# Performance work log

Measured on AMD Instinct MI355X. Metric: run time of the kernel, lower is better.

Reference implementation:

```python
import jax, jax.numpy as jnp
import numpy as np

IN_FEATURES = 4096
OUT_FEATURES = 11008
GROUP_SIZE = 128
N_HIGH = 1024   # int(0.25*4096)//8*8
N_LOW = 3072    # (4096-1024)//8*8
M_TOKENS = 64


def unpack_6bit(packed, original_k):
    # packed: [K*3//4, N] uint8 values stored as int32
    _, N = packed.shape
    p = packed.reshape(original_k // 4, 3, N)
    b0, b1, b2 = p[:, 0], p[:, 1], p[:, 2]
    v0 = b0 & 63
    v1 = ((b0 >> 6) & 3) | ((b1 & 15) << 2)
    v2 = ((b1 >> 4) & 15) | ((b2 & 3) << 4)
    v3 = (b2 >> 2) & 63
    return jnp.stack([v0, v1, v2, v3], axis=1).reshape(original_k, N)


def unpack_5bit(packed, original_k):
    # packed: [K*5//8, N]
    _, N = packed.shape
    p = packed.reshape(original_k // 8, 5, N)
    b = [p[:, i] for i in range(5)]
    v0 = b[0] & 31
    v1 = ((b[0] >> 5) & 7) | ((b[1] & 3) << 3)
    v2 = (b[1] >> 2) & 31
    v3 = ((b[1] >> 7) & 1) | ((b[2] & 15) << 1)
    v4 = ((b[2] >> 4) & 15) | ((b[3] & 1) << 4)
    v5 = (b[3] >> 1) & 31
    v6 = ((b[3] >> 6) & 3) | ((b[4] & 7) << 2)
    v7 = (b[4] >> 3) & 31
    return jnp.stack([v0, v1, v2, v3, v4, v5, v6, v7], axis=1).reshape(original_k, N)


def dequant_region(W_q, scales, half_range):
    # W_q: [K, N] ints in [0, 2*half_range]; scales: [num_groups, N]
    K, N = W_q.shape
    G = scales.shape[0]
    Wg = (W_q.astype(jnp.float32) - float(half_range)).reshape(G, GROUP_SIZE, N)
    return (Wg * scales[:, None, :]).reshape(K, N)


def setup_inputs() -> dict:
    key = jax.random.key(0)
    ks = jax.random.split(key, 7)
    x = jax.random.normal(ks[0], (M_TOKENS, IN_FEATURES), dtype=jnp.float32)
    W_high_packed = jax.random.randint(ks[1], (N_HIGH * 3 // 4, OUT_FEATURES), 0, 256, dtype=jnp.int32)
    W_low_packed = jax.random.randint(ks[2], (N_LOW * 5 // 8, OUT_FEATURES), 0, 256, dtype=jnp.int32)
    scales_high = jax.random.uniform(ks[3], (N_HIGH // GROUP_SIZE, OUT_FEATURES), dtype=jnp.float32) * 0.02 + 1e-4
    scales_low = jax.random.uniform(ks[4], (N_LOW // GROUP_SIZE, OUT_FEATURES), dtype=jnp.float32) * 0.02 + 1e-4
    col_indices = jax.random.permutation(ks[5], IN_FEATURES).astype(jnp.int32)
    bias = jax.random.normal(ks[6], (OUT_FEATURES,), dtype=jnp.float32) * 0.02
    return {"x": x, "W_high_packed": W_high_packed, "W_low_packed": W_low_packed,
            "scales_high": scales_high, "scales_low": scales_low,
            "col_indices": col_indices, "bias": bias}


def reference(x, W_high_packed, W_low_packed, scales_high, scales_low, col_indices, bias):
    # Unpack mixed 6-bit / 5-bit weights and group-dequantize.
    Wq_high = unpack_6bit(W_high_packed, N_HIGH)          # [1024, N], 0..63
    Wq_low = unpack_5bit(W_low_packed, N_LOW)             # [3072, N], 0..31
    W_high = dequant_region(Wq_high, scales_high, 31)     # 6-bit half_range = 31
    W_low = dequant_region(Wq_low, scales_low, 15)        # 5-bit half_range = 15
    # Column-sensitivity reorder of activations, then split high/low regions.
    x_perm = x[:, col_indices]                            # [M, K]
    x_high = x_perm[:, :N_HIGH]
    x_low = x_perm[:, N_HIGH:N_HIGH + N_LOW]
    out = x_high @ W_high + x_low @ W_low + bias          # [M, N]
    return out
```

## Files before the change

kernel.cpp:

```cpp
#include <hip/hip_runtime.h>


#define NFEAT 11008
#define KTOT  4096

typedef _Float16 half8 __attribute__((ext_vector_type(8)));
typedef float    f32x4 __attribute__((ext_vector_type(4)));

#define GLOAD4(g, l)  __builtin_amdgcn_global_load_lds(                         \
    (const __attribute__((address_space(1))) unsigned int*)(g),                 \
    (__attribute__((address_space(3))) unsigned int*)(l), 4, 0, 0)
#define GLOAD16(g, l) __builtin_amdgcn_global_load_lds(                         \
    (const __attribute__((address_space(1))) unsigned int*)(g),                 \
    (__attribute__((address_space(3))) unsigned int*)(l), 16, 0, 0)
#define WAITV(N) asm volatile("s_waitcnt vmcnt(" #N ")" ::: "memory")

__global__ __launch_bounds__(256) void prep_xfrag(const float* __restrict__ x,
                                                  const int* __restrict__ col,
                                                  _Float16* __restrict__ xfrag) {
    int idx = blockIdx.x * 256 + threadIdx.x;
    int j  = idx & 7;
    int l  = (idx >> 3) & 63;
    int mt = (idx >> 9) & 3;
    int s  = idx >> 11;
    int k  = s * 32 + ((l >> 4) << 3) + j;
    int m  = mt * 16 + (l & 15);
    xfrag[idx] = (_Float16)x[m * KTOT + col[k]];
}

__global__ __launch_bounds__(256, 3) void gemm_kernel(const int* __restrict__ Wh,
                                                      const int* __restrict__ Wl,
                                                      const float* __restrict__ sh,
                                                      const float* __restrict__ sl,
                                                      const _Float16* __restrict__ xfrag,
                                                      float* __restrict__ dst,
                                                      int atomic_mode) {
    const int n0   = blockIdx.x * 64;
    const int kc   = blockIdx.y;
    const int lane = threadIdx.x & 63;
    const int wave = threadIdx.x >> 6;
    const int cb   = wave * 16 + (lane & 15);
    const int n    = n0 + cb;
    const int o    = lane >> 4;

    __shared__ int Wb[4][1632];
    __shared__ __align__(16) _Float16 Ab[4][4][512];

    f32x4 acc[4];
#pragma unroll
    for (int i = 0; i < 4; ++i) acc[i] = (f32x4){0.f, 0.f, 0.f, 0.f};

    if (kc == 0) {
        float sc[8];
#pragma unroll
        for (int g = 0; g < 8; ++g) sc[g] = sh[g * NFEAT + n];

#define STAGE6(T) do {                                                         \
        const int _t = (T); const int _b = _t & 3;                             \
        const int* _gs = Wh + (_t * 24 + wave * 6) * NFEAT + n0 + lane;        \
        GLOAD4(_gs,             &Wb[_b][(wave * 6 + 0) * 68]);                 \
        GLOAD4(_gs + 1 * NFEAT, &Wb[_b][(wave * 6 + 1) * 68]);                 \
        GLOAD4(_gs + 2 * NFEAT, &Wb[_b][(wave * 6 + 2) * 68]);                 \
        GLOAD4(_gs + 3 * NFEAT, &Wb[_b][(wave * 6 + 3) * 68]);                 \
        GLOAD4(_gs + 4 * NFEAT, &Wb[_b][(wave * 6 + 4) * 68]);                 \
        GLOAD4(_gs + 5 * NFEAT, &Wb[_b][(wave * 6 + 5) * 68]);                 \
        GLOAD16(xfrag + ((size_t)(_t * 4 + wave) * 64 + lane) * 8,             \
                &Ab[_b][wave][0]);                                             \
    } while (0)

        STAGE6(0);
        STAGE6(1);
#pragma unroll
        for (int g = 0; g < 8; ++g) {
            for (int st = 0; st < 4; ++st) {
                const int t = g * 4 + st;
                if (t + 2 < 32) { STAGE6(t + 2); WAITV(14); }
                else if (t + 1 < 32) { WAITV(7); }
                else { WAITV(0); }
                __builtin_amdgcn_s_barrier();
                asm volatile("" ::: "memory");

                const int  bi = t & 3;
                const int* wr = &Wb[bi][(o * 6) * 68 + cb];
                const int b0 = wr[0];      const int b1 = wr[68];
                const int b2 = wr[2 * 68]; const int b3 = wr[3 * 68];
                const int b4 = wr[4 * 68]; const int b5 = wr[5 * 68];
                int v0 = b0 & 63;
                int v1 = ((b0 >> 6) & 3) | ((b1 & 15) << 2);
                int v2 = ((b1 >> 4) & 15) | ((b2 & 3) << 4);
                int v3 = (b2 >> 2) & 63;
                int v4 = b3 & 63;
                int v5 = ((b3 >> 6) & 3) | ((b4 & 15) << 2);
                int v6 = ((b4 >> 4) & 15) | ((b5 & 3) << 4);
                int v7 = (b5 >> 2) & 63;
                const float s = sc[g], moff = -31.0f * sc[g];
                half8 bf;
                bf[0] = (_Float16)fmaf((float)v0, s, moff);
                bf[1] = (_Float16)fmaf((float)v1, s, moff);
                bf[2] = (_Float16)fmaf((float)v2, s, moff);
                bf[3] = (_Float16)fmaf((float)v3, s, moff);
                bf[4] = (_Float16)fmaf((float)v4, s, moff);
                bf[5] = (_Float16)fmaf((float)v5, s, moff);
                bf[6] = (_Float16)fmaf((float)v6, s, moff);
                bf[7] = (_Float16)fmaf((float)v7, s, moff);
#pragma unroll
                for (int mt = 0; mt < 4; ++mt) {
                    half8 a = *(const half8*)&Ab[bi][mt][lane * 8];
                    acc[mt] = __builtin_amdgcn_mfma_f32_16x16x32_f16(a, bf, acc[mt], 0, 0, 0);
                }
            }
        }
#undef STAGE6
    } else {
        const int klc   = kc - 1;
        const int rbase = klc * 640;
        float sc[8];
#pragma unroll
        for (int g = 0; g < 8; ++g) sc[g] = sl[(klc * 8 + g) * NFEAT + n];

#define STAGE5(T) do {                                                         \
        const int _t = (T); const int _b = _t & 3;                             \
        const int* _gs = Wl + (rbase + _t * 20 + wave * 5) * NFEAT + n0 + lane;\
        GLOAD4(_gs,             &Wb[_b][(wave * 5 + 0) * 72]);                 \
        GLOAD4(_gs + 1 * NFEAT, &Wb[_b][(wave * 5 + 1) * 72]);                 \
        GLOAD4(_gs + 2 * NFEAT, &Wb[_b][(wave * 5 + 2) * 72]);                 \
        GLOAD4(_gs + 3 * NFEAT, &Wb[_b][(wave * 5 + 3) * 72]);                 \
        GLOAD4(_gs + 4 * NFEAT, &Wb[_b][(wave * 5 + 4) * 72]);                 \
        GLOAD16(xfrag + ((size_t)((kc * 32 + _t) * 4 + wave) * 64 + lane) * 8, \
                &Ab[_b][wave][0]);                                             \
    } while (0)

        STAGE5(0);
        STAGE5(1);
#pragma unroll
        for (int g = 0; g < 8; ++g) {
            for (int st = 0; st < 4; ++st) {
                const int t = g * 4 + st;
                if (t + 2 < 32) { STAGE5(t + 2); WAITV(12); }
                else if (t + 1 < 32) { WAITV(6); }
                else { WAITV(0); }
                __builtin_amdgcn_s_barrier();
                asm volatile("" ::: "memory");

                const int  bi = t & 3;
                const int* wr = &Wb[bi][(o * 5) * 72 + cb];
                const int b0 = wr[0];      const int b1 = wr[72];
                const int b2 = wr[2 * 72]; const int b3 = wr[3 * 72];
                const int b4 = wr[4 * 72];
                int v0 = b0 & 31;
                int v1 = ((b0 >> 5) & 7) | ((b1 & 3) << 3);
                int v2 = (b1 >> 2) & 31;
                int v3 = ((b1 >> 7) & 1) | ((b2 & 15) << 1);
                int v4 = ((b2 >> 4) & 15) | ((b3 & 1) << 4);
                int v5 = (b3 >> 1) & 31;
                int v6 = ((b3 >> 6) & 3) | ((b4 & 7) << 2);
                int v7 = (b4 >> 3) & 31;
                const float s = sc[g], moff = -15.0f * sc[g];
                half8 bf;
                bf[0] = (_Float16)fmaf((float)v0, s, moff);
                bf[1] = (_Float16)fmaf((float)v1, s, moff);
                bf[2] = (_Float16)fmaf((float)v2, s, moff);
                bf[3] = (_Float16)fmaf((float)v3, s, moff);
                bf[4] = (_Float16)fmaf((float)v4, s, moff);
                bf[5] = (_Float16)fmaf((float)v5, s, moff);
                bf[6] = (_Float16)fmaf((float)v6, s, moff);
                bf[7] = (_Float16)fmaf((float)v7, s, moff);
#pragma unroll
                for (int mt = 0; mt < 4; ++mt) {
                    half8 a = *(const half8*)&Ab[bi][mt][lane * 8];
                    acc[mt] = __builtin_amdgcn_mfma_f32_16x16x32_f16(a, bf, acc[mt], 0, 0, 0);
                }
            }
        }
#undef STAGE5
    }

    const int r0 = (lane >> 4) << 2;
    if (atomic_mode) {
#pragma unroll
        for (int mt = 0; mt < 4; ++mt)
#pragma unroll
            for (int r = 0; r < 4; ++r)
                atomicAdd(&dst[(mt * 16 + r0 + r) * NFEAT + n], acc[mt][r]);
    } else {
        float* base = dst + (size_t)kc * 64 * NFEAT;
#pragma unroll
        for (int mt = 0; mt < 4; ++mt)
#pragma unroll
            for (int r = 0; r < 4; ++r)
                base[(mt * 16 + r0 + r) * NFEAT + n] = acc[mt][r];
    }
}

__global__ __launch_bounds__(256) void reduce_out(const float* __restrict__ part,
                                                  const float* __restrict__ bias,
                                                  float* __restrict__ out, int nc) {
    const int idx = blockIdx.x * 256 + threadIdx.x;
    const int f   = idx * 4;
    const int n   = f % NFEAT;
    f32x4 sum = *(const f32x4*)(bias + n);
    for (int c = 0; c < nc; ++c)
        sum += *(const f32x4*)(part + (size_t)c * 704512 + f);
    *(f32x4*)(out + f) = sum;
}

__global__ __launch_bounds__(256) void init_bias(const float* __restrict__ bias,
                                                 float* __restrict__ out) {
    const int idx = blockIdx.x * 256 + threadIdx.x;
    out[idx] = bias[idx % NFEAT];
}

extern "C" void kernel_launch(void* const* d_in, const int* in_sizes, int n_in,
                              void* d_out, int out_size, void* d_ws, size_t ws_size,
                              hipStream_t stream) {
    const float* x    = (const float*)d_in[0];
    const int*   Wh   = (const int*)d_in[1];
    const int*   Wl   = (const int*)d_in[2];
    const float* sh   = (const float*)d_in[3];
    const float* sl   = (const float*)d_in[4];
    const int*   col  = (const int*)d_in[5];
    const float* bias = (const float*)d_in[6];
    float* out = (float*)d_out;

    _Float16* xfrag = (_Float16*)d_ws;
    const size_t xfrag_bytes = 64 * KTOT * sizeof(_Float16);
    const size_t part1 = 64ull * NFEAT * sizeof(float);

    prep_xfrag<<<1024, 256, 0, stream>>>(x, col, xfrag);

    dim3 grid(172, 4);
    if (ws_size >= xfrag_bytes + 4 * part1) {
        float* part = (float*)((char*)d_ws + xfrag_bytes);
        gemm_kernel<<<grid, 256, 0, stream>>>(Wh, Wl, sh, sl, xfrag, part, 0);
        reduce_out<<<688, 256, 0, stream>>>(part, bias, out, 4);
    } else {
        init_bias<<<2752, 256, 0, stream>>>(bias, out);
        gemm_kernel<<<grid, 256, 0, stream>>>(Wh, Wl, sh, sl, xfrag, out, 1);
    }
}
```

Measured before the change: 173.0 us.

## Widen N tile to 128, use 16-byte LDS loads, split K into eight chunks

Each block now covers 128 output columns and a 512-wide K chunk, giving a grid of 86x8 instead of 172x4. Weight rows are staged with 16-byte global-to-LDS loads rather than 4-byte ones, and the LDS ring shrinks to a triple buffer with the barrier placed before the next stage is issued. Each wave now computes two N sub-tiles, so every A fragment read from LDS feeds twice as many MFMAs. The cost is twice as many partial-sum planes for the reduction pass and more accumulator registers, which may lower occupancy.

```diff
diff --git a/kernel.cpp b/kernel.cpp
--- a/kernel.cpp
+++ b/kernel.cpp
@@ -7,13 +7,11 @@
 typedef _Float16 half8 __attribute__((ext_vector_type(8)));
 typedef float    f32x4 __attribute__((ext_vector_type(4)));
 
-#define GLOAD4(g, l)  __builtin_amdgcn_global_load_lds(                         \
-    (const __attribute__((address_space(1))) unsigned int*)(g),                 \
-    (__attribute__((address_space(3))) unsigned int*)(l), 4, 0, 0)
 #define GLOAD16(g, l) __builtin_amdgcn_global_load_lds(                         \
     (const __attribute__((address_space(1))) unsigned int*)(g),                 \
     (__attribute__((address_space(3))) unsigned int*)(l), 16, 0, 0)
 #define WAITV(N) asm volatile("s_waitcnt vmcnt(" #N ")" ::: "memory")
+#define FENCE()  asm volatile("" ::: "memory")
 
 __global__ __launch_bounds__(256) void prep_xfrag(const float* __restrict__ x,
                                                   const int* __restrict__ col,
@@ -35,56 +33,65 @@
                                                       const _Float16* __restrict__ xfrag,
                                                       float* __restrict__ dst,
                                                       int atomic_mode) {
-    const int n0   = blockIdx.x * 64;
+    const int bx   = blockIdx.x;
     const int kc   = blockIdx.y;
     const int lane = threadIdx.x & 63;
     const int wave = threadIdx.x >> 6;
-    const int cb   = wave * 16 + (lane & 15);
-    const int n    = n0 + cb;
+    const int n0   = bx * 128;
     const int o    = lane >> 4;
-
-    __shared__ int Wb[4][1632];
-    __shared__ __align__(16) _Float16 Ab[4][4][512];
-
-    f32x4 acc[4];
-#pragma unroll
-    for (int i = 0; i < 4; ++i) acc[i] = (f32x4){0.f, 0.f, 0.f, 0.f};
-
-    if (kc == 0) {
-        float sc[8];
-#pragma unroll
-        for (int g = 0; g < 8; ++g) sc[g] = sh[g * NFEAT + n];
-
-#define STAGE6(T) do {                                                         \
-        const int _t = (T); const int _b = _t & 3;                             \
-        const int* _gs = Wh + (_t * 24 + wave * 6) * NFEAT + n0 + lane;        \
-        GLOAD4(_gs,             &Wb[_b][(wave * 6 + 0) * 68]);                 \
-        GLOAD4(_gs + 1 * NFEAT, &Wb[_b][(wave * 6 + 1) * 68]);                 \
-        GLOAD4(_gs + 2 * NFEAT, &Wb[_b][(wave * 6 + 2) * 68]);                 \
-        GLOAD4(_gs + 3 * NFEAT, &Wb[_b][(wave * 6 + 3) * 68]);                 \
-        GLOAD4(_gs + 4 * NFEAT, &Wb[_b][(wave * 6 + 4) * 68]);                 \
-        GLOAD4(_gs + 5 * NFEAT, &Wb[_b][(wave * 6 + 5) * 68]);                 \
-        GLOAD16(xfrag + ((size_t)(_t * 4 + wave) * 64 + lane) * 8,             \
-                &Ab[_b][wave][0]);                                             \
+    const int c0   = wave * 32 + (lane & 15);
+    const int rsub = lane >> 5;
+    const int coff = (lane & 31) * 4;
+
+    __shared__ int Wb[3][12 * 264];
+    __shared__ __align__(16) _Float16 Ab[3][4][512];
+
+    f32x4 acc[4][2];
+#pragma unroll
+    for (int i = 0; i < 4; ++i)
+#pragma unroll
+        for (int j = 0; j < 2; ++j) acc[i][j] = (f32x4){0.f, 0.f, 0.f, 0.f};
+
+    if (kc < 2) {
+        const int k0    = kc * 512;
+        const int rbase = 3 * (k0 >> 2);
+        float sc[4][2];
+#pragma unroll
+        for (int g = 0; g < 4; ++g)
+#pragma unroll
+            for (int nt = 0; nt < 2; ++nt)
+                sc[g][nt] = sh[((k0 >> 7) + g) * NFEAT + n0 + c0 + nt * 16];
+
+#define STAGE6(T, BUF) do {                                                     \
+        const int _rb = rbase + (T) * 24;                                       \
+        _Pragma("unroll")                                                       \
+        for (int _i = 0; _i < 3; ++_i) {                                        \
+            const int _p = 3 * wave + _i;                                       \
+            GLOAD16(Wh + (size_t)(_rb + 2 * _p + rsub) * NFEAT + n0 + coff,     \
+                    &Wb[BUF][_p * 264]);                                        \
+        }                                                                       \
+        GLOAD16(xfrag + ((size_t)((kc * 16 + (T)) * 4 + wave) * 64 + lane) * 8, \
+                &Ab[BUF][wave][0]);                                             \
     } while (0)
 
-        STAGE6(0);
-        STAGE6(1);
-#pragma unroll
-        for (int g = 0; g < 8; ++g) {
-            for (int st = 0; st < 4; ++st) {
-                const int t = g * 4 + st;
-                if (t + 2 < 32) { STAGE6(t + 2); WAITV(14); }
-                else if (t + 1 < 32) { WAITV(7); }
-                else { WAITV(0); }
-                __builtin_amdgcn_s_barrier();
-                asm volatile("" ::: "memory");
-
-                const int  bi = t & 3;
-                const int* wr = &Wb[bi][(o * 6) * 68 + cb];
-                const int b0 = wr[0];      const int b1 = wr[68];
-                const int b2 = wr[2 * 68]; const int b3 = wr[3 * 68];
-                const int b4 = wr[4 * 68]; const int b5 = wr[5 * 68];
+        STAGE6(0, 0);
+        STAGE6(1, 1);
+#pragma unroll
+        for (int t = 0; t < 16; ++t) {
+            if (t < 15) { WAITV(4); } else { WAITV(0); }
+            __builtin_amdgcn_s_barrier();
+            FENCE();
+            if (t + 2 < 16) STAGE6(t + 2, (t + 2) % 3);
+            const int bi = t % 3;
+#pragma unroll
+            for (int nt = 0; nt < 2; ++nt) {
+                const int c = c0 + nt * 16;
+                const int b0 = Wb[bi][(3 * o + 0) * 264 +   0 + c];
+                const int b1 = Wb[bi][(3 * o + 0) * 264 + 128 + c];
+                const int b2 = Wb[bi][(3 * o + 1) * 264 +   0 + c];
+                const int b3 = Wb[bi][(3 * o + 1) * 264 + 128 + c];
+                const int b4 = Wb[bi][(3 * o + 2) * 264 +   0 + c];
+                const int b5 = Wb[bi][(3 * o + 2) * 264 + 128 + c];
                 int v0 = b0 & 63;
                 int v1 = ((b0 >> 6) & 3) | ((b1 & 15) << 2);
                 int v2 = ((b1 >> 4) & 15) | ((b2 & 3) << 4);
@@ -93,7 +100,7 @@
                 int v5 = ((b3 >> 6) & 3) | ((b4 & 15) << 2);
                 int v6 = ((b4 >> 4) & 15) | ((b5 & 3) << 4);
                 int v7 = (b5 >> 2) & 63;
-                const float s = sc[g], moff = -31.0f * sc[g];
+                const float s = sc[t >> 2][nt], moff = -31.0f * s;
                 half8 bf;
                 bf[0] = (_Float16)fmaf((float)v0, s, moff);
                 bf[1] = (_Float16)fmaf((float)v1, s, moff);
@@ -106,47 +113,55 @@
 #pragma unroll
                 for (int mt = 0; mt < 4; ++mt) {
                     half8 a = *(const half8*)&Ab[bi][mt][lane * 8];
-                    acc[mt] = __builtin_amdgcn_mfma_f32_16x16x32_f16(a, bf, acc[mt], 0, 0, 0);
+                    acc[mt][nt] = __builtin_amdgcn_mfma_f32_16x16x32_f16(a, bf, acc[mt][nt], 0, 0, 0);
                 }
             }
         }
 #undef STAGE6
     } else {
-        const int klc   = kc - 1;
-        const int rbase = klc * 640;
-        float sc[8];
-#pragma unroll
-        for (int g = 0; g < 8; ++g) sc[g] = sl[(klc * 8 + g) * NFEAT + n];
-
-#define STAGE5(T) do {                                                         \
-        const int _t = (T); const int _b = _t & 3;                             \
-        const int* _gs = Wl + (rbase + _t * 20 + wave * 5) * NFEAT + n0 + lane;\
-        GLOAD4(_gs,             &Wb[_b][(wave * 5 + 0) * 72]);                 \
-        GLOAD4(_gs + 1 * NFEAT, &Wb[_b][(wave * 5 + 1) * 72]);                 \
-        GLOAD4(_gs + 2 * NFEAT, &Wb[_b][(wave * 5 + 2) * 72]);                 \
-        GLOAD4(_gs + 3 * NFEAT, &Wb[_b][(wave * 5 + 3) * 72]);                 \
-        GLOAD4(_gs + 4 * NFEAT, &Wb[_b][(wave * 5 + 4) * 72]);                 \
-        GLOAD16(xfrag + ((size_t)((kc * 32 + _t) * 4 + wave) * 64 + lane) * 8, \
-                &Ab[_b][wave][0]);                                             \
+        const int kl0   = (kc - 2) * 512;
+        const int rbase = 5 * (kl0 >> 3);
+        float sc[4][2];
+#pragma unroll
+        for (int g = 0; g < 4; ++g)
+#pragma unroll
+            for (int nt = 0; nt < 2; ++nt)
+                sc[g][nt] = sl[((kl0 >> 7) + g) * NFEAT + n0 + c0 + nt * 16];
+
+        const int npair = (wave < 2) ? 3 : 2;
+        const int pbase = (wave < 2) ? 3 * wave : 2 * wave + 2;
+
+#define STAGE5(T, BUF) do {                                                     \
+        const int _rb = rbase + (T) * 20;                                       \
+        for (int _i = 0; _i < npair; ++_i) {                                    \
+            const int _p = pbase + _i;                                          \
+            GLOAD16(Wl + (size_t)(_rb + 2 * _p + rsub) * NFEAT + n0 + coff,     \
+                    &Wb[BUF][_p * 264]);                                        \
+        }                                                                       \
+        GLOAD16(xfrag + ((size_t)((kc * 16 + (T)) * 4 + wave) * 64 + lane) * 8, \
+                &Ab[BUF][wave][0]);                                             \
     } while (0)
 
-        STAGE5(0);
-        STAGE5(1);
-#pragma unroll
-        for (int g = 0; g < 8; ++g) {
-            for (int st = 0; st < 4; ++st) {
-                const int t = g * 4 + st;
-                if (t + 2 < 32) { STAGE5(t + 2); WAITV(12); }
-                else if (t + 1 < 32) { WAITV(6); }
-                else { WAITV(0); }
-                __builtin_amdgcn_s_barrier();
-                asm volatile("" ::: "memory");
-
-                const int  bi = t & 3;
-                const int* wr = &Wb[bi][(o * 5) * 72 + cb];
-                const int b0 = wr[0];      const int b1 = wr[72];
-                const int b2 = wr[2 * 72]; const int b3 = wr[3 * 72];
-                const int b4 = wr[4 * 72];
+        STAGE5(0, 0);
+        STAGE5(1, 1);
+#pragma unroll
+        for (int t = 0; t < 16; ++t) {
+            if (t < 15) {
+                if (wave < 2) { WAITV(4); } else { WAITV(3); }
+            } else { WAITV(0); }
+            __builtin_amdgcn_s_barrier();
+            FENCE();
+            if (t + 2 < 16) STAGE5(t + 2, (t + 2) % 3);
+            const int bi = t % 3;
+#pragma unroll
+            for (int nt = 0; nt < 2; ++nt) {
+                const int c = c0 + nt * 16;
+                const int r0i = 5 * o;
+                const int b0 = Wb[bi][((r0i + 0) >> 1) * 264 + ((r0i + 0) & 1) * 128 + c];
+                const int b1 = Wb[bi][((r0i + 1) >> 1) * 264 + ((r0i + 1) & 1) * 128 + c];
+                const int b2 = Wb[bi][((r0i + 2) >> 1) * 264 + ((r0i + 2) & 1) * 128 + c];
+                const int b3 = Wb[bi][((r0i + 3) >> 1) * 264 + ((r0i + 3) & 1) * 128 + c];
+                const int b4 = Wb[bi][((r0i + 4) >> 1) * 264 + ((r0i + 4) & 1) * 128 + c];
                 int v0 = b0 & 31;
                 int v1 = ((b0 >> 5) & 7) | ((b1 & 3) << 3);
                 int v2 = (b1 >> 2) & 31;
@@ -155,7 +170,7 @@
                 int v5 = (b3 >> 1) & 31;
                 int v6 = ((b3 >> 6) & 3) | ((b4 & 7) << 2);
                 int v7 = (b4 >> 3) & 31;
-                const float s = sc[g], moff = -15.0f * sc[g];
+                const float s = sc[t >> 2][nt], moff = -15.0f * s;
                 half8 bf;
                 bf[0] = (_Float16)fmaf((float)v0, s, moff);
                 bf[1] = (_Float16)fmaf((float)v1, s, moff);
@@ -168,7 +183,7 @@
 #pragma unroll
                 for (int mt = 0; mt < 4; ++mt) {
                     half8 a = *(const half8*)&Ab[bi][mt][lane * 8];
-                    acc[mt] = __builtin_amdgcn_mfma_f32_16x16x32_f16(a, bf, acc[mt], 0, 0, 0);
+                    acc[mt][nt] = __builtin_amdgcn_mfma_f32_16x16x32_f16(a, bf, acc[mt][nt], 0, 0, 0);
                 }
             }
         }
@@ -180,15 +195,19 @@
 #pragma unroll
         for (int mt = 0; mt < 4; ++mt)
 #pragma unroll
-            for (int r = 0; r < 4; ++r)
-                atomicAdd(&dst[(mt * 16 + r0 + r) * NFEAT + n], acc[mt][r]);
+            for (int nt = 0; nt < 2; ++nt)
+#pragma unroll
+                for (int r = 0; r < 4; ++r)
+                    atomicAdd(&dst[(mt * 16 + r0 + r) * NFEAT + n0 + c0 + nt * 16], acc[mt][nt][r]);
     } else {
         float* base = dst + (size_t)kc * 64 * NFEAT;
 #pragma unroll
         for (int mt = 0; mt < 4; ++mt)
 #pragma unroll
-            for (int r = 0; r < 4; ++r)
-                base[(mt * 16 + r0 + r) * NFEAT + n] = acc[mt][r];
+            for (int nt = 0; nt < 2; ++nt)
+#pragma unroll
+                for (int r = 0; r < 4; ++r)
+                    base[(mt * 16 + r0 + r) * NFEAT + n0 + c0 + nt * 16] = acc[mt][nt][r];
     }
 }
 
@@ -228,11 +247,11 @@
 
     prep_xfrag<<<1024, 256, 0, stream>>>(x, col, xfrag);
 
-    dim3 grid(172, 4);
-    if (ws_size >= xfrag_bytes + 4 * part1) {
+    dim3 grid(86, 8);
+    if (ws_size >= xfrag_bytes + 8 * part1) {
         float* part = (float*)((char*)d_ws + xfrag_bytes);
         gemm_kernel<<<grid, 256, 0, stream>>>(Wh, Wl, sh, sl, xfrag, part, 0);
-        reduce_out<<<688, 256, 0, stream>>>(part, bias, out, 4);
+        reduce_out<<<688, 256, 0, stream>>>(part, bias, out, 8);
     } else {
         init_bias<<<2752, 256, 0, stream>>>(bias, out);
         gemm_kernel<<<grid, 256, 0, stream>>>(Wh, Wl, sh, sl, xfrag, out, 1);
```

Measured after the change: 177.1 us. 2.4% more time.
